# Optimization experiments

Hardware: AMD Instinct MI355X
Metric: run time of the kernel (lower is better)

The kernel has to match this reference:

```python
import jax, jax.numpy as jnp
import numpy as np

INPUT_DIM = 1024
HIDDEN_DIM = 1024
FORGET_BIAS = 0.0


def setup_inputs() -> dict:
    key = jax.random.key(0)
    ks = jax.random.split(key, 8)
    x = jax.random.normal(ks[0], (1024, 32, INPUT_DIM), dtype=jnp.float32)
    state = jnp.zeros((1, 32, HIDDEN_DIM), dtype=jnp.float32)
    std = 0.1
    wm_z = std * jax.random.normal(ks[1], (HIDDEN_DIM, INPUT_DIM), dtype=jnp.float32)
    wm_f = std * jax.random.normal(ks[2], (HIDDEN_DIM, INPUT_DIM), dtype=jnp.float32)
    wv_z = std * jax.random.normal(ks[3], (1, HIDDEN_DIM), dtype=jnp.float32)
    wv_f = std * jax.random.normal(ks[4], (1, HIDDEN_DIM), dtype=jnp.float32)
    bias_z = std * jax.random.normal(ks[5], (1, HIDDEN_DIM), dtype=jnp.float32)
    bias_f = std * jax.random.normal(ks[6], (1, HIDDEN_DIM), dtype=jnp.float32) + FORGET_BIAS
    return {"x": x, "state": state, "wm_z": wm_z, "wm_f": wm_f,
            "wv_z": wv_z, "wv_f": wv_f, "bias_z": bias_z, "bias_f": bias_f}


def reference(x, state, wm_z, wm_f, wv_z, wv_f, bias_z, bias_f):
    # x: [slen, bsz, in_dim]; state: [1, bsz, hidden]
    hidden_prev = state[0]  # [bsz, hidden]
    # Pre-activation input projections (batched GEMM over all timesteps).
    out_z = jnp.einsum('sbi,hi->sbh', x, wm_z)  # [slen, bsz, hidden]
    out_f = jnp.einsum('sbi,hi->sbh', x, wm_f)

    def step(cell, zf):
        z_, f_ = zf
        z_part = jnp.tanh(z_ + wv_z * cell + bias_z)
        f_part = jax.nn.sigmoid(f_ + wv_f * cell + bias_f)
        new_cell = cell * f_part + (1.0 - f_part) * z_part
        return new_cell, new_cell

    _, new_cells = jax.lax.scan(step, hidden_prev, (out_z, out_f))
    return new_cells  # [slen, bsz, hidden]
```

## Files before the change

kernel.cpp:

```cpp
#include <hip/hip_runtime.h>
#include <hip/hip_fp16.h>

#define S_LEN 1024
#define BSZ   32
#define IN_DIM 1024
#define HID   1024
#define MDIM  (S_LEN*BSZ)
#define NDIM  (2*HID)
#define KDIM  IN_DIM

typedef __attribute__((ext_vector_type(8))) _Float16 half8;
typedef __attribute__((ext_vector_type(2))) _Float16 half2v;
typedef __attribute__((ext_vector_type(4))) float    floatx4;

__global__ void cvt_x_kernel(const float* __restrict__ x, _Float16* __restrict__ xh) {
    int idx = blockIdx.x * blockDim.x + threadIdx.x;
    const float4* src = (const float4*)x + (size_t)idx * 2;
    float4 a = src[0], b = src[1];
    half8 h;
    h[0] = (_Float16)a.x; h[1] = (_Float16)a.y; h[2] = (_Float16)a.z; h[3] = (_Float16)a.w;
    h[4] = (_Float16)b.x; h[5] = (_Float16)b.y; h[6] = (_Float16)b.z; h[7] = (_Float16)b.w;
    *((half8*)xh + idx) = h;
}

__global__ void cvt_w_kernel(const float* __restrict__ wz, const float* __restrict__ wf,
                             _Float16* __restrict__ wh) {
    int idx = blockIdx.x * blockDim.x + threadIdx.x;
    int e0 = idx * 8;
    int r   = e0 >> 10;
    int col = e0 & 1023;
    int g = r >> 5, sub = r & 31;
    const float* src = (sub < 16)
        ? wz + ((size_t)(g * 16 + sub)      * KDIM + col)
        : wf + ((size_t)(g * 16 + sub - 16) * KDIM + col);
    const float4* s4 = (const float4*)src;
    float4 a = s4[0], b = s4[1];
    half8 h;
    h[0] = (_Float16)a.x; h[1] = (_Float16)a.y; h[2] = (_Float16)a.z; h[3] = (_Float16)a.w;
    h[4] = (_Float16)b.x; h[5] = (_Float16)b.y; h[6] = (_Float16)b.z; h[7] = (_Float16)b.w;
    *((half8*)wh + idx) = h;
}

#define BM 256
#define BN 256
#define BK 64
#define TPB 4
#define NGT (TPB * 16)
#define NIT (NGT / 2)

__global__ __launch_bounds__(512, 2) void gemm_f16_kernel(
    const _Float16* __restrict__ A, const _Float16* __restrict__ B,
    uint* __restrict__ zf) {
    __shared__ __attribute__((aligned(128))) _Float16 smem[65536];
    char* smb = (char*)smem;

    const int tid  = threadIdx.x;
    const int lane = tid & 63;
    const int wv   = tid >> 6;
    const int wm_off = (wv >> 2) * 128;
    const int wn_off = (wv & 3) * 64;

    const int n0g  = (blockIdx.x & 7) * BN;
    const int m_bs = (blockIdx.x >> 3) * (TPB * BM);

    const int fr  = lane & 15;
    const int fkb = (lane >> 4) * 16;

    const int srow = lane >> 3;
    const int skb  = ((lane & 7) ^ srow) << 4;

    floatx4 acc[8][4] = {};

    auto STAGE_A = [&](int g, int R0) {
        int kt = g & 15, mt = (g >> 4) & 3;
        int r = R0 + wv * 8 + srow;
        const _Float16* gp = A + (size_t)(m_bs + mt * BM + r) * KDIM + kt * BK + (skb >> 1);
        __builtin_amdgcn_global_load_lds(
            (const __attribute__((address_space(1))) void*)gp,
            (__attribute__((address_space(3))) void*)(smb + (g & 1) * 65536 + (R0 + wv * 8) * 128),
            16, 0, 0);
    };
    auto STAGE_B = [&](int g, int R0) {
        int kt = g & 15;
        int r = R0 + wv * 8 + srow;
        const _Float16* gp = B + (size_t)(n0g + r) * KDIM + kt * BK + (skb >> 1);
        __builtin_amdgcn_global_load_lds(
            (const __attribute__((address_space(1))) void*)gp,
            (__attribute__((address_space(3))) void*)(smb + (g & 1) * 65536 + 32768 + (R0 + wv * 8) * 128),
            16, 0, 0);
    };
    auto LD8 = [&](int rb, int r, int kb) -> half8 {
        return *(const half8*)(smb + rb + r * 128 + (kb ^ ((r & 7) << 4)));
    };

    STAGE_B(0, 0);   STAGE_B(0, 64);
    STAGE_A(0, 0);   STAGE_A(0, 128);
    STAGE_B(0, 128); STAGE_B(0, 192);
    STAGE_A(0, 64);  STAGE_A(0, 192);
    STAGE_B(1, 0);   STAGE_B(1, 64);
    STAGE_A(1, 0);   STAGE_A(1, 128);
    STAGE_B(1, 128); STAGE_B(1, 192);
    asm volatile("s_waitcnt vmcnt(6)" ::: "memory");
    __builtin_amdgcn_s_barrier();
    asm volatile("" ::: "memory");

    half8 bfr[4][2];
    for (int it = 0; it < NIT; ++it) {
        const int  t    = 2 * it;
        const bool more = (it < NIT - 1);
        #pragma unroll
        for (int ph = 0; ph < 8; ++ph) {
            const int bb    = ph >> 2;
            const int p     = ph & 3;
            const int bbase = bb * 65536;

            if (p == 0) {
                #pragma unroll
                for (int j = 0; j < 4; ++j)
                    #pragma unroll
                    for (int ks = 0; ks < 2; ++ks) {
                        int r = wn_off + j * 16 + fr;
                        bfr[j][ks] = LD8(bbase + 32768, r, ks * 64 + fkb);
                    }
            }
            half8 afr[2][2];
            #pragma unroll
            for (int ii = 0; ii < 2; ++ii)
                #pragma unroll
                for (int ks = 0; ks < 2; ++ks) {
                    int r = wm_off + (2 * p + ii) * 16 + fr;
                    afr[ii][ks] = LD8(bbase, r, ks * 64 + fkb);
                }

            if (ph == 0) {
                STAGE_A(t + 1, 64);  STAGE_A(t + 1, 192);
            } else if (more) {
                if      (ph == 1) { STAGE_B(t + 2, 0);   STAGE_B(t + 2, 64);  }
                else if (ph == 2) { STAGE_A(t + 2, 0);   STAGE_A(t + 2, 128); }
                else if (ph == 3) { STAGE_B(t + 2, 128); STAGE_B(t + 2, 192); }
                else if (ph == 4) { STAGE_A(t + 2, 64);  STAGE_A(t + 2, 192); }
                else if (ph == 5) { STAGE_B(t + 3, 0);   STAGE_B(t + 3, 64);  }
                else if (ph == 6) { STAGE_A(t + 3, 0);   STAGE_A(t + 3, 128); }
                else              { STAGE_B(t + 3, 128); STAGE_B(t + 3, 192); }
            }

            __builtin_amdgcn_s_barrier();
            asm volatile("s_waitcnt lgkmcnt(0)" ::: "memory");
            __builtin_amdgcn_s_setprio(1);
            #pragma unroll
            for (int ks = 0; ks < 2; ++ks)
                #pragma unroll
                for (int ii = 0; ii < 2; ++ii)
                    #pragma unroll
                    for (int j = 0; j < 4; ++j)
                        acc[2 * p + ii][j] = __builtin_amdgcn_mfma_f32_16x16x32_f16(
                            afr[ii][ks], bfr[j][ks], acc[2 * p + ii][j], 0, 0, 0);
            __builtin_amdgcn_s_setprio(0);
            if (ph == 3) {
                if (more) asm volatile("s_waitcnt vmcnt(6)" ::: "memory");
                else      asm volatile("s_waitcnt vmcnt(0)" ::: "memory");
            } else if (ph == 7) {
                if (more) asm volatile("s_waitcnt vmcnt(6)" ::: "memory");
            }
            __builtin_amdgcn_s_barrier();
            asm volatile("" ::: "memory");
        }

        if ((it & 7) == 7) {
            const int m0   = m_bs + (it >> 3) * BM;
            const int orow = (lane >> 4) * 4;
            const int ocol = lane & 15;
            const int gb   = (n0g + wn_off) >> 5;
            #pragma unroll
            for (int i = 0; i < 8; ++i)
                #pragma unroll
                for (int p2 = 0; p2 < 2; ++p2) {
                    int hh = (gb + p2) * 16 + ocol;
                    #pragma unroll
                    for (int r = 0; r < 4; ++r) {
                        int row = m0 + wm_off + i * 16 + orow + r;
                        half2v v;
                        v[0] = (_Float16)acc[i][2 * p2][r];
                        v[1] = (_Float16)acc[i][2 * p2 + 1][r];
                        *(half2v*)(zf + (size_t)row * HID + hh) = v;
                    }
                }
            #pragma unroll
            for (int i = 0; i < 8; ++i)
                #pragma unroll
                for (int j = 0; j < 4; ++j)
                    acc[i][j] = (floatx4)0.0f;
        }
    }
}

#define UNR 32
__device__ __forceinline__ float fast_exp2(float x) {
    float r;
    asm("v_exp_f32 %0, %1" : "=v"(r) : "v"(x));
    return r;
}
__global__ __launch_bounds__(64) void scan_kernel(
    const uint* __restrict__ zf, float* __restrict__ out,
    const float* __restrict__ state,
    const float* __restrict__ wvz, const float* __restrict__ wvf,
    const float* __restrict__ bz, const float* __restrict__ bfv) {
    const int t = blockIdx.x * 64 + threadIdx.x;
    const int h = t & (HID - 1);
    const int stride = BSZ * HID;

    float cell = state[t];
    const float L2E = 1.44269504088896f;
    const float azt = 2.0f * L2E * wvz[h];
    const float czt = 2.0f * L2E * bz[h];
    const float aft = -L2E * wvf[h];
    const float cft = -L2E * bfv[h];

    const uint* p = zf + t;
    float* po = out + t;

    uint buf[UNR];
    #pragma unroll
    for (int u = 0; u < UNR; ++u) buf[u] = p[(size_t)u * stride];

    for (int s0 = 0; s0 < S_LEN; s0 += UNR) {
        uint nb[UNR];
        if (s0 + UNR < S_LEN) {
            #pragma unroll
            for (int u = 0; u < UNR; ++u)
                nb[u] = p[(size_t)(s0 + UNR + u) * stride];
        }
        #pragma unroll
        for (int u = 0; u < UNR; ++u) {
            half2v h2 = __builtin_bit_cast(half2v, buf[u]);
            float zb = fmaf((float)h2[0], 2.0f * L2E, czt);
            float fb = fmaf((float)h2[1], -L2E, cft);
            float ez = fast_exp2(fmaf(azt, cell, zb));
            float zp = fmaf(-2.0f, __builtin_amdgcn_rcpf(ez + 1.0f), 1.0f);
            float ef = fast_exp2(fmaf(aft, cell, fb));
            float fp = __builtin_amdgcn_rcpf(ef + 1.0f);
            cell = fmaf(cell - zp, fp, zp);
            po[(size_t)(s0 + u) * stride] = cell;
        }
        #pragma unroll
        for (int u = 0; u < UNR; ++u) buf[u] = nb[u];
    }
}

extern "C" void kernel_launch(void* const* d_in, const int* in_sizes, int n_in,
                              void* d_out, int out_size, void* d_ws, size_t ws_size,
                              hipStream_t stream) {
    const float* x      = (const float*)d_in[0];
    const float* state  = (const float*)d_in[1];
    const float* wm_z   = (const float*)d_in[2];
    const float* wm_f   = (const float*)d_in[3];
    const float* wv_z   = (const float*)d_in[4];
    const float* wv_f   = (const float*)d_in[5];
    const float* bias_z = (const float*)d_in[6];
    const float* bias_f = (const float*)d_in[7];
    float* out = (float*)d_out;

    char* ws = (char*)d_ws;
    _Float16* xh = (_Float16*)ws;
    _Float16* wh = (_Float16*)(ws + (size_t)MDIM * KDIM * sizeof(_Float16));
    uint* zf     = (uint*)(ws + (size_t)MDIM * KDIM * sizeof(_Float16)
                              + (size_t)NDIM * KDIM * sizeof(_Float16));

    cvt_x_kernel<<<(MDIM * KDIM) / (256 * 8), 256, 0, stream>>>(x, xh);
    cvt_w_kernel<<<(NDIM * KDIM) / (256 * 8), 256, 0, stream>>>(wm_z, wm_f, wh);

    gemm_f16_kernel<<<256, 512, 0, stream>>>(xh, wh, zf);

    scan_kernel<<<MDIM / 64, 64, 0, stream>>>(zf, out, state, wv_z, wv_f, bias_z, bias_f);
}
```

Measured before the change: 425.1 us.

## Merge conversion kernels, remap GEMM block order, double-buffer A fragments

```diff
diff --git a/kernel.cpp b/kernel.cpp
--- a/kernel.cpp
+++ b/kernel.cpp
@@ -9,36 +9,37 @@
 #define NDIM  (2*HID)
 #define KDIM  IN_DIM
 
-typedef __attribute__((ext_vector_type(8))) _Float16 half8;
-typedef __attribute__((ext_vector_type(2))) _Float16 half2v;
-typedef __attribute__((ext_vector_type(4))) float    floatx4;
-
-__global__ void cvt_x_kernel(const float* __restrict__ x, _Float16* __restrict__ xh) {
+typedef __attribute__((ext_vector_type(8)))  _Float16 half8;
+typedef __attribute__((ext_vector_type(2)))  _Float16 half2v;
+typedef __attribute__((ext_vector_type(4)))  float    floatx4;
+
+#define NXV ((MDIM*KDIM)/8)
+__global__ void cvt_xw_kernel(const float* __restrict__ x,
+                              const float* __restrict__ wz, const float* __restrict__ wf,
+                              _Float16* __restrict__ xh, _Float16* __restrict__ wh) {
     int idx = blockIdx.x * blockDim.x + threadIdx.x;
-    const float4* src = (const float4*)x + (size_t)idx * 2;
-    float4 a = src[0], b = src[1];
-    half8 h;
-    h[0] = (_Float16)a.x; h[1] = (_Float16)a.y; h[2] = (_Float16)a.z; h[3] = (_Float16)a.w;
-    h[4] = (_Float16)b.x; h[5] = (_Float16)b.y; h[6] = (_Float16)b.z; h[7] = (_Float16)b.w;
-    *((half8*)xh + idx) = h;
-}
-
-__global__ void cvt_w_kernel(const float* __restrict__ wz, const float* __restrict__ wf,
-                             _Float16* __restrict__ wh) {
-    int idx = blockIdx.x * blockDim.x + threadIdx.x;
-    int e0 = idx * 8;
-    int r   = e0 >> 10;
-    int col = e0 & 1023;
-    int g = r >> 5, sub = r & 31;
-    const float* src = (sub < 16)
-        ? wz + ((size_t)(g * 16 + sub)      * KDIM + col)
-        : wf + ((size_t)(g * 16 + sub - 16) * KDIM + col);
-    const float4* s4 = (const float4*)src;
+    const float4* s4;
+    half8* dst;
+    if (idx < NXV) {
+        s4 = (const float4*)x + (size_t)idx * 2;
+        dst = (half8*)xh + idx;
+    } else {
+        int wi = idx - NXV;
+        int e0 = wi * 8;
+        int r   = e0 >> 10;
+        int col = e0 & 1023;
+        int g = r >> 5, sub = r & 31;
+        const float* src = (sub < 16)
+            ? wz + ((size_t)(g * 16 + sub)      * KDIM + col)
+            : wf + ((size_t)(g * 16 + sub - 16) * KDIM + col);
+        s4 = (const float4*)src;
+        dst = (half8*)wh + wi;
+    }
     float4 a = s4[0], b = s4[1];
     half8 h;
     h[0] = (_Float16)a.x; h[1] = (_Float16)a.y; h[2] = (_Float16)a.z; h[3] = (_Float16)a.w;
     h[4] = (_Float16)b.x; h[5] = (_Float16)b.y; h[6] = (_Float16)b.z; h[7] = (_Float16)b.w;
-    *((half8*)wh + idx) = h;
+    *dst = h;
 }
 
 #define BM 256
@@ -60,8 +61,10 @@
     const int wm_off = (wv >> 2) * 128;
     const int wn_off = (wv & 3) * 64;
 
-    const int n0g  = (blockIdx.x & 7) * BN;
-    const int m_bs = (blockIdx.x >> 3) * (TPB * BM);
+    const int b      = blockIdx.x;
+    const int mchunk = (b & 7) + 8 * ((b >> 3) & 3);
+    const int m_bs   = mchunk * (TPB * BM);
+    const int n0g    = (b >> 5) * BN;
 
     const int fr  = lane & 15;
     const int fkb = (lane >> 4) * 16;
@@ -105,32 +108,41 @@
     asm volatile("" ::: "memory");
 
     half8 bfr[4][2];
+    half8 afrA[2][2], afrB[2][2];
     for (int it = 0; it < NIT; ++it) {
         const int  t    = 2 * it;
         const bool more = (it < NIT - 1);
         #pragma unroll
         for (int ph = 0; ph < 8; ++ph) {
-            const int bb    = ph >> 2;
-            const int p     = ph & 3;
-            const int bbase = bb * 65536;
-
-            if (p == 0) {
+            const int q     = ph & 3;
+            const int bbase = (ph >> 2) * 65536;
+
+            if (q == 0) {
                 #pragma unroll
                 for (int j = 0; j < 4; ++j)
                     #pragma unroll
+                    for (int ks = 0; ks < 2; ++ks)
+                        bfr[j][ks] = LD8(bbase + 32768, wn_off + j * 16 + fr, ks * 64 + fkb);
+                #pragma unroll
+                for (int ii = 0; ii < 2; ++ii)
+                    #pragma unroll
                     for (int ks = 0; ks < 2; ++ks) {
-                        int r = wn_off + j * 16 + fr;
-                        bfr[j][ks] = LD8(bbase + 32768, r, ks * 64 + fkb);
+                        afrA[ii][ks] = LD8(bbase, wm_off + ii * 16 + fr,        ks * 64 + fkb);
+                        afrB[ii][ks] = LD8(bbase, wm_off + (2 + ii) * 16 + fr,  ks * 64 + fkb);
                     }
-            }
-            half8 afr[2][2];
-            #pragma unroll
-            for (int ii = 0; ii < 2; ++ii)
-                #pragma unroll
-                for (int ks = 0; ks < 2; ++ks) {
-                    int r = wm_off + (2 * p + ii) * 16 + fr;
-                    afr[ii][ks] = LD8(bbase, r, ks * 64 + fkb);
-                }
+            } else if (q == 1) {
+                #pragma unroll
+                for (int ii = 0; ii < 2; ++ii)
+                    #pragma unroll
+                    for (int ks = 0; ks < 2; ++ks)
+                        afrA[ii][ks] = LD8(bbase, wm_off + (4 + ii) * 16 + fr, ks * 64 + fkb);
+            } else if (q == 2) {
+                #pragma unroll
+                for (int ii = 0; ii < 2; ++ii)
+                    #pragma unroll
+                    for (int ks = 0; ks < 2; ++ks)
+                        afrB[ii][ks] = LD8(bbase, wm_off + (6 + ii) * 16 + fr, ks * 64 + fkb);
+            }
 
             if (ph == 0) {
                 STAGE_A(t + 1, 64);  STAGE_A(t + 1, 192);
@@ -145,16 +157,27 @@
             }
 
             __builtin_amdgcn_s_barrier();
-            asm volatile("s_waitcnt lgkmcnt(0)" ::: "memory");
+            asm volatile("" ::: "memory");
             __builtin_amdgcn_s_setprio(1);
-            #pragma unroll
-            for (int ks = 0; ks < 2; ++ks)
-                #pragma unroll
-                for (int ii = 0; ii < 2; ++ii)
-                    #pragma unroll
-                    for (int j = 0; j < 4; ++j)
-                        acc[2 * p + ii][j] = __builtin_amdgcn_mfma_f32_16x16x32_f16(
-                            afr[ii][ks], bfr[j][ks], acc[2 * p + ii][j], 0, 0, 0);
+            if (q == 0 || q == 2) {
+                #pragma unroll
+                for (int ks = 0; ks < 2; ++ks)
+                    #pragma unroll
+                    for (int ii = 0; ii < 2; ++ii)
+                        #pragma unroll
+                        for (int j = 0; j < 4; ++j)
+                            acc[2 * q + ii][j] = __builtin_amdgcn_mfma_f32_16x16x32_f16(
+                                afrA[ii][ks], bfr[j][ks], acc[2 * q + ii][j], 0, 0, 0);
+            } else {
+                #pragma unroll
+                for (int ks = 0; ks < 2; ++ks)
+                    #pragma unroll
+                    for (int ii = 0; ii < 2; ++ii)
+                        #pragma unroll
+                        for (int j = 0; j < 4; ++j)
+                            acc[2 * q + ii][j] = __builtin_amdgcn_mfma_f32_16x16x32_f16(
+                                afrB[ii][ks], bfr[j][ks], acc[2 * q + ii][j], 0, 0, 0);
+            }
             __builtin_amdgcn_s_setprio(0);
             if (ph == 3) {
                 if (more) asm volatile("s_waitcnt vmcnt(6)" ::: "memory");
@@ -266,8 +289,8 @@
     uint* zf     = (uint*)(ws + (size_t)MDIM * KDIM * sizeof(_Float16)
                               + (size_t)NDIM * KDIM * sizeof(_Float16));
 
-    cvt_x_kernel<<<(MDIM * KDIM) / (256 * 8), 256, 0, stream>>>(x, xh);
-    cvt_w_kernel<<<(NDIM * KDIM) / (256 * 8), 256, 0, stream>>>(wm_z, wm_f, wh);
+    cvt_xw_kernel<<<((MDIM + NDIM) * KDIM) / (256 * 8), 256, 0, stream>>>(
+        x, wm_z, wm_f, xh, wh);
 
     gemm_f16_kernel<<<256, 512, 0, stream>>>(xh, wh, zf);
 
```

After: 430.5 us. Within noise of the previous version (+1.3%).
